# Optimization experiments

Measured on AMD Instinct MI355X. Metric: run time of the kernel, lower is better.

Reference implementation:

```python
import jax, jax.numpy as jnp
import numpy as np

ALPHA = 2.0    # ATan surrogate sharpness
V_TH = 1.0     # LIF firing threshold
TAU = 2.0      # LIF membrane time constant
BN_EPS = 1e-5
NUM_HEADS = 8

@jax.custom_vjp
def spike(u):
    return (u >= 0.0).astype(u.dtype)

def _spike_fwd(u):
    return spike(u), u

def _spike_bwd(u, g):
    s = (jnp.pi / 2.0) * ALPHA * u
    return (g * (ALPHA / 2.0) / (1.0 + s * s),)

spike.defvjp(_spike_fwd, _spike_bwd)

def lif(x):
    # x: (T, ...) -> binary spikes, multi-step LIF with hard reset
    def step(mem, xt):
        mem = mem + (xt - mem) / TAU
        s = spike(mem - V_TH)
        return mem * (1.0 - s), s
    _, out = jax.lax.scan(step, jnp.zeros_like(x[0]), x)
    return out

def bn_eval(y, bn):
    g, be, m, v = bn[0], bn[1], bn[2], bn[3]  # each (C,)
    return (y - m) * jax.lax.rsqrt(v + BN_EPS) * g + be

def linear_bn_lif(x, W, b, bn):
    # x: (T,B,N,C); W: (C_out, C_in) torch convention
    y = jnp.einsum('tbnc,dc->tbnd', x, W) + b
    return lif(bn_eval(y, bn))

def setup_inputs() -> dict:
    key = jax.random.key(0)
    ks = jax.random.split(key, 6)
    T, B, N, C = 4, 8, 1024, 512
    scale = 1.0 / np.sqrt(C)
    x = jax.random.normal(ks[0], (T, B, N, C), dtype=jnp.float32)
    Wq = jax.random.normal(ks[1], (C, C), dtype=jnp.float32) * scale
    Wk = jax.random.normal(ks[2], (C, C), dtype=jnp.float32) * scale
    Wv = jax.random.normal(ks[3], (C, C), dtype=jnp.float32) * scale
    Wp = jax.random.normal(ks[4], (C, C), dtype=jnp.float32) * scale
    zeros = jnp.zeros((C,), dtype=jnp.float32)
    ones = jnp.ones((C,), dtype=jnp.float32)
    # bn_params[l] = (gamma, beta, running_mean, running_var) for q_bn,k_bn,v_bn,proj_bn
    bn_one = jnp.stack([ones, zeros, zeros, ones])  # (4, C)
    bn_params = jnp.tile(bn_one[None], (4, 1, 1))   # (4, 4, C)
    return {"x": x, "Wq": Wq, "bq": zeros, "Wk": Wk, "bk": zeros,
            "Wv": Wv, "bv": zeros, "Wp": Wp, "bp": zeros, "bn_params": bn_params}

def reference(x, Wq, bq, Wk, bk, Wv, bv, Wp, bp, bn_params):
    T, B, N, C = x.shape
    H = NUM_HEADS
    D = C // H
    q = linear_bn_lif(x, Wq, bq, bn_params[0])
    k = linear_bn_lif(x, Wk, bk, bn_params[1])
    v = linear_bn_lif(x, Wv, bv, bn_params[2])
    # (T,B,N,C) -> (T,B,H,N,D)
    q = q.reshape(T, B, N, H, D).transpose(0, 1, 3, 2, 4)
    k = k.reshape(T, B, N, H, D).transpose(0, 1, 3, 2, 4)
    v = v.reshape(T, B, N, H, D).transpose(0, 1, 3, 2, 4)
    # attention_linear variant: kv = (k^T @ v) / n; y = q @ kv
    # SparseMatmul's tile-sparsity fallback computes the same dense matmul math.
    kv = jnp.einsum('tbhnd,tbhne->tbhde', k, v) / float(N)
    y = jnp.einsum('tbhnd,tbhde->tbhne', q, kv)
    y = y.transpose(0, 1, 3, 2, 4).reshape(T, B, N, C)
    y = lif(y)  # attn_lif
    # final projection: proj -> proj_bn -> proj_lif
    y = jnp.einsum('tbnc,dc->tbnd', y, Wp) + bp
    y = bn_eval(y, bn_params[3])
    y = lif(y)  # proj_lif
    return y
```

## Files before the change

kernel.cpp:

```cpp
#include <hip/hip_runtime.h>
#include <hip/hip_bf16.h>

constexpr int T_ = 4, B_ = 8, N_ = 1024, C_ = 512, H_ = 8, D_ = 64;
constexpr int M_ = B_ * N_;
constexpr int MT_ = T_ * M_;
constexpr int K_ = 512;

#define TAU_INV 0.5f
#define V_TH    1.0f
#define BN_EPS  1e-5f

__device__ __forceinline__ void ld4(const float* p, float* d) {
  const float4 v = *(const float4*)p;
  d[0] = v.x; d[1] = v.y; d[2] = v.z; d[3] = v.w;
}
__device__ __forceinline__ void ld4(const __hip_bfloat16* p, float* d) {
  const ushort4 u = *(const ushort4*)p;
  d[0] = __bfloat162float(*(const __hip_bfloat16*)&u.x);
  d[1] = __bfloat162float(*(const __hip_bfloat16*)&u.y);
  d[2] = __bfloat162float(*(const __hip_bfloat16*)&u.z);
  d[3] = __bfloat162float(*(const __hip_bfloat16*)&u.w);
}
__device__ __forceinline__ void st4(__hip_bfloat16* p, const float* s) {
  ushort4 u;
  *(__hip_bfloat16*)&u.x = __float2bfloat16(s[0]);
  *(__hip_bfloat16*)&u.y = __float2bfloat16(s[1]);
  *(__hip_bfloat16*)&u.z = __float2bfloat16(s[2]);
  *(__hip_bfloat16*)&u.w = __float2bfloat16(s[3]);
  *(ushort4*)p = u;
}
__device__ __forceinline__ void st4(float* p, const float* s) {
  *(float4*)p = make_float4(s[0], s[1], s[2], s[3]);
}

template <typename TIn>
__global__ __launch_bounds__(256, 2) void gemm_bn(
    const TIn* __restrict__ A, const float* __restrict__ W,
    const float* __restrict__ bias, const float* __restrict__ bnp,
    float* __restrict__ Y)
{
  constexpr int BK = 32;
  __shared__ __align__(16) float As[BK][128 + 4];
  __shared__ __align__(16) float Bs[BK][256 + 8];

  const int tid = threadIdx.x;
  const int tx = tid & 15, ty = tid >> 4;
  const int bm = blockIdx.y * 128;
  const int bn0 = blockIdx.x * 256;

  float acc[2][4][4][4];
#pragma unroll
  for (int g = 0; g < 2; ++g)
#pragma unroll
    for (int h = 0; h < 4; ++h)
#pragma unroll
      for (int i = 0; i < 4; ++i)
#pragma unroll
        for (int j = 0; j < 4; ++j) acc[g][h][i][j] = 0.0f;

  for (int k0 = 0; k0 < K_; k0 += BK) {
#pragma unroll
    for (int i = 0; i < 4; ++i) {
      const int idx = tid + 256 * i;
      const int row = idx >> 3, q = idx & 7;
      float tmp[4];
      ld4(&A[(size_t)(bm + row) * K_ + k0 + q * 4], tmp);
#pragma unroll
      for (int j = 0; j < 4; ++j) As[q * 4 + j][row] = tmp[j];
    }
#pragma unroll
    for (int i = 0; i < 8; ++i) {
      const int idx = tid + 256 * i;
      const int n = idx >> 3, q = idx & 7;
      float tmp[4];
      ld4(&W[(size_t)(bn0 + n) * K_ + k0 + q * 4], tmp);
#pragma unroll
      for (int j = 0; j < 4; ++j) Bs[q * 4 + j][n] = tmp[j];
    }
    __syncthreads();

#pragma unroll
    for (int kk = 0; kk < BK; ++kk) {
      float a[2][4], b[4][4];
#pragma unroll
      for (int g = 0; g < 2; ++g)
        ld4(&As[kk][ty * 4 + g * 64], a[g]);
#pragma unroll
      for (int h = 0; h < 4; ++h)
        ld4(&Bs[kk][tx * 4 + h * 64], b[h]);
#pragma unroll
      for (int g = 0; g < 2; ++g)
#pragma unroll
        for (int h = 0; h < 4; ++h)
#pragma unroll
          for (int i = 0; i < 4; ++i)
#pragma unroll
            for (int j = 0; j < 4; ++j)
              acc[g][h][i][j] += a[g][i] * b[h][j];
    }
    __syncthreads();
  }

#pragma unroll
  for (int h = 0; h < 4; ++h) {
    const int dl = tx * 4 + h * 64;
    const int d = bn0 + dl;
    float bi[4], gg[4], be[4], mu[4], vv[4];
    ld4(&bias[d], bi);
    ld4(&bnp[d], gg);
    ld4(&bnp[C_ + d], be);
    ld4(&bnp[2 * C_ + d], mu);
    ld4(&bnp[3 * C_ + d], vv);
    float inv[4];
#pragma unroll
    for (int j = 0; j < 4; ++j) inv[j] = 1.0f / sqrtf(vv[j] + BN_EPS);
#pragma unroll
    for (int g = 0; g < 2; ++g)
#pragma unroll
      for (int i = 0; i < 4; ++i) {
        const int row = bm + ty * 4 + g * 64 + i;
        float sv[4];
#pragma unroll
        for (int j = 0; j < 4; ++j) {
          float y = acc[g][h][i][j] + bi[j];
          y = (y - mu[j]) * inv[j] * gg[j] + be[j];
          sv[j] = y;
        }
        st4(&Y[(size_t)row * C_ + d], sv);
      }
  }
}

template <typename TOut>
__global__ __launch_bounds__(256) void lif_scan(
    const float* __restrict__ Y, TOut* __restrict__ S)
{
  const size_t npt = (size_t)M_ * C_;
  const size_t idx4 = ((size_t)blockIdx.x * 256 + threadIdx.x) * 4;
  if (idx4 >= npt) return;
  float mem[4] = {0.0f, 0.0f, 0.0f, 0.0f};
#pragma unroll
  for (int t = 0; t < T_; ++t) {
    float y[4], sv[4];
    ld4(&Y[(size_t)t * npt + idx4], y);
#pragma unroll
    for (int j = 0; j < 4; ++j) {
      float m2 = mem[j] + (y[j] - mem[j]) * TAU_INV;
      float s = (m2 - V_TH >= 0.0f) ? 1.0f : 0.0f;
      sv[j] = s;
      mem[j] = (s != 0.0f) ? 0.0f : m2;
    }
    st4(&S[(size_t)t * npt + idx4], sv);
  }
}

__global__ __launch_bounds__(256) void attn_kernel(
    const __hip_bfloat16* __restrict__ Q,
    const __hip_bfloat16* __restrict__ Kk,
    const __hip_bfloat16* __restrict__ V,
    float* __restrict__ Y)
{
  __shared__ float s1[64][65];
  __shared__ float s2[64][65];
  __shared__ float kv[64][65];
  const int tid = threadIdx.x;
  const int h = blockIdx.x, b = blockIdx.y, t = blockIdx.z;
  const size_t base = ((size_t)t * B_ + b) * (size_t)N_ * C_ + (size_t)h * D_;
  const int d0 = (tid >> 4) * 4;
  const int e0 = (tid & 15) * 4;

  float acc[4][4];
#pragma unroll
  for (int i = 0; i < 4; ++i)
#pragma unroll
    for (int j = 0; j < 4; ++j) acc[i][j] = 0.0f;

  for (int nc = 0; nc < N_; nc += 64) {
#pragma unroll
    for (int i = 0; i < 16; ++i) {
      int idx = tid + i * 256;
      int r = idx >> 6, c = idx & 63;
      s1[r][c] = __bfloat162float(Kk[base + (size_t)(nc + r) * C_ + c]);
      s2[r][c] = __bfloat162float(V[base + (size_t)(nc + r) * C_ + c]);
    }
    __syncthreads();
#pragma unroll
    for (int nn = 0; nn < 64; ++nn) {
      float a[4], bb[4];
#pragma unroll
      for (int i = 0; i < 4; ++i) a[i] = s1[nn][d0 + i];
#pragma unroll
      for (int j = 0; j < 4; ++j) bb[j] = s2[nn][e0 + j];
#pragma unroll
      for (int i = 0; i < 4; ++i)
#pragma unroll
        for (int j = 0; j < 4; ++j) acc[i][j] += a[i] * bb[j];
    }
    __syncthreads();
  }
#pragma unroll
  for (int i = 0; i < 4; ++i)
#pragma unroll
    for (int j = 0; j < 4; ++j)
      kv[d0 + i][e0 + j] = acc[i][j] * (1.0f / (float)N_);
  __syncthreads();

  for (int rc = 0; rc < N_; rc += 64) {
#pragma unroll
    for (int i = 0; i < 16; ++i) {
      int idx = tid + i * 256;
      int r = idx >> 6, c = idx & 63;
      s1[r][c] = __bfloat162float(Q[base + (size_t)(rc + r) * C_ + c]);
    }
    __syncthreads();
    float o[4][4];
#pragma unroll
    for (int i = 0; i < 4; ++i)
#pragma unroll
      for (int j = 0; j < 4; ++j) o[i][j] = 0.0f;
#pragma unroll
    for (int d = 0; d < 64; ++d) {
      float a[4], bb[4];
#pragma unroll
      for (int i = 0; i < 4; ++i) a[i] = s1[d0 + i][d];
#pragma unroll
      for (int j = 0; j < 4; ++j) bb[j] = kv[d][e0 + j];
#pragma unroll
      for (int i = 0; i < 4; ++i)
#pragma unroll
        for (int j = 0; j < 4; ++j) o[i][j] += a[i] * bb[j];
    }
#pragma unroll
    for (int i = 0; i < 4; ++i)
#pragma unroll
      for (int j = 0; j < 4; ++j)
        Y[base + (size_t)(rc + d0 + i) * C_ + e0 + j] = o[i][j];
    __syncthreads();
  }
}

extern "C" void kernel_launch(void* const* d_in, const int* in_sizes, int n_in,
                              void* d_out, int out_size, void* d_ws, size_t ws_size,
                              hipStream_t stream)
{
  const float* x   = (const float*)d_in[0];
  const float* Wq  = (const float*)d_in[1];
  const float* bq  = (const float*)d_in[2];
  const float* Wk  = (const float*)d_in[3];
  const float* bk  = (const float*)d_in[4];
  const float* Wv  = (const float*)d_in[5];
  const float* bv  = (const float*)d_in[6];
  const float* Wp  = (const float*)d_in[7];
  const float* bp  = (const float*)d_in[8];
  const float* bnp = (const float*)d_in[9];
  float* out = (float*)d_out;

  char* ws = (char*)d_ws;
  const size_t nElem = (size_t)T_ * M_ * C_;
  float*          Y   = (float*)ws;          ws += nElem * sizeof(float);
  __hip_bfloat16* q_s = (__hip_bfloat16*)ws; ws += nElem * sizeof(__hip_bfloat16);
  __hip_bfloat16* k_s = (__hip_bfloat16*)ws; ws += nElem * sizeof(__hip_bfloat16);
  __hip_bfloat16* v_s = (__hip_bfloat16*)ws; ws += nElem * sizeof(__hip_bfloat16);
  __hip_bfloat16* a_s = (__hip_bfloat16*)ws; ws += nElem * sizeof(__hip_bfloat16);

  const dim3 gg(C_ / 256, MT_ / 128);
  const unsigned lif_grid = (unsigned)(((size_t)M_ * C_ / 4 + 255) / 256);

  gemm_bn<float><<<gg, 256, 0, stream>>>(x, Wq, bq, bnp + 0 * 4 * C_, Y);
  lif_scan<__hip_bfloat16><<<lif_grid, 256, 0, stream>>>(Y, q_s);
  gemm_bn<float><<<gg, 256, 0, stream>>>(x, Wk, bk, bnp + 1 * 4 * C_, Y);
  lif_scan<__hip_bfloat16><<<lif_grid, 256, 0, stream>>>(Y, k_s);
  gemm_bn<float><<<gg, 256, 0, stream>>>(x, Wv, bv, bnp + 2 * 4 * C_, Y);
  lif_scan<__hip_bfloat16><<<lif_grid, 256, 0, stream>>>(Y, v_s);

  attn_kernel<<<dim3(H_, B_, T_), 256, 0, stream>>>(q_s, k_s, v_s, Y);
  lif_scan<__hip_bfloat16><<<lif_grid, 256, 0, stream>>>(Y, a_s);

  gemm_bn<__hip_bfloat16><<<gg, 256, 0, stream>>>(a_s, Wp, bp, bnp + 3 * 4 * C_, Y);
  lif_scan<float><<<lif_grid, 256, 0, stream>>>(Y, out);
}
```

Measured before the change: 1.178 ms.

## Batch Q/K/V GEMMs into one launch over row halves with swizzled shared tiles

The Q, K and V projections now run as one GEMM launch, with blockIdx.z picking the weight, done in two halves over the M rows so the float staging buffer stays smaller. A fused LIF kernel then scans all three outputs per half. The GEMM tile K depth drops from 32 to 16 with an XOR swizzle on the shared-memory column layout to cut bank conflicts, and launch bounds allow 3 blocks per SM. This cuts the number of launches and improves occupancy and x reuse across the three weights. The cost is a larger workspace (3x half-size Y) and more K-loop iterations with syncs.

```diff
diff --git a/kernel.cpp b/kernel.cpp
--- a/kernel.cpp
+++ b/kernel.cpp
@@ -3,8 +3,8 @@
 
 constexpr int T_ = 4, B_ = 8, N_ = 1024, C_ = 512, H_ = 8, D_ = 64;
 constexpr int M_ = B_ * N_;
-constexpr int MT_ = T_ * M_;
 constexpr int K_ = 512;
+constexpr int MH_ = 4096;
 
 #define TAU_INV 0.5f
 #define V_TH    1.0f
@@ -33,21 +33,39 @@
   *(float4*)p = make_float4(s[0], s[1], s[2], s[3]);
 }
 
-template <typename TIn>
-__global__ __launch_bounds__(256, 2) void gemm_bn(
-    const TIn* __restrict__ A, const float* __restrict__ W,
-    const float* __restrict__ bias, const float* __restrict__ bnp,
-    float* __restrict__ Y)
-{
-  constexpr int BK = 32;
-  __shared__ __align__(16) float As[BK][128 + 4];
-  __shared__ __align__(16) float Bs[BK][256 + 8];
+template <typename TIn> struct GemmArgs {
+  const TIn* A;
+  const float* W[3];
+  const float* bias[3];
+  const float* bn[3];
+  float* Y[3];
+  int half_base;
+};
+
+template <int RSHIFT, typename TIn>
+__global__ __launch_bounds__(256, 3) void gemm_bn(GemmArgs<TIn> args)
+{
+  constexpr int BK = 16;
+  constexpr int RMASK = (1 << RSHIFT) - 1;
+  __shared__ __align__(16) float AsF[BK * 132];
+  __shared__ __align__(16) float BsF[BK * 260];
+
+  const int w = blockIdx.z;
+  const TIn*   __restrict__ A    = args.A;
+  const float* __restrict__ W    = args.W[w];
+  const float* __restrict__ bias = args.bias[w];
+  const float* __restrict__ bnp  = args.bn[w];
+  float*       __restrict__ Y    = args.Y[w];
+  const int halfb = args.half_base;
 
   const int tid = threadIdx.x;
   const int tx = tid & 15, ty = tid >> 4;
   const int bm = blockIdx.y * 128;
   const int bn0 = blockIdx.x * 256;
 
+  const float* Ard[2] = { AsF + (ty ^ 0) * 4, AsF + (ty ^ 1) * 4 };
+  const float* Brd[2] = { BsF + (tx ^ 0) * 4, BsF + (tx ^ 1) * 4 };
+
   float acc[2][4][4][4];
 #pragma unroll
   for (int g = 0; g < 2; ++g)
@@ -59,35 +77,40 @@
         for (int j = 0; j < 4; ++j) acc[g][h][i][j] = 0.0f;
 
   for (int k0 = 0; k0 < K_; k0 += BK) {
+#pragma unroll
+    for (int i = 0; i < 2; ++i) {
+      const int idx = tid + 256 * i;
+      const int m = idx >> 2, q = idx & 3;
+      const int r = bm + m;
+      const size_t arow = (size_t)(r >> RSHIFT) * M_ + halfb + (r & RMASK);
+      float tmp[4];
+      ld4(&A[arow * K_ + k0 + q * 4], tmp);
+      const int colb = (((m >> 2) ^ (q >> 1)) << 2) + (m & 3);
+#pragma unroll
+      for (int j = 0; j < 4; ++j) AsF[(4 * q + j) * 132 + colb] = tmp[j];
+    }
 #pragma unroll
     for (int i = 0; i < 4; ++i) {
       const int idx = tid + 256 * i;
-      const int row = idx >> 3, q = idx & 7;
-      float tmp[4];
-      ld4(&A[(size_t)(bm + row) * K_ + k0 + q * 4], tmp);
-#pragma unroll
-      for (int j = 0; j < 4; ++j) As[q * 4 + j][row] = tmp[j];
-    }
-#pragma unroll
-    for (int i = 0; i < 8; ++i) {
-      const int idx = tid + 256 * i;
-      const int n = idx >> 3, q = idx & 7;
+      const int n = idx >> 2, q = idx & 3;
       float tmp[4];
       ld4(&W[(size_t)(bn0 + n) * K_ + k0 + q * 4], tmp);
-#pragma unroll
-      for (int j = 0; j < 4; ++j) Bs[q * 4 + j][n] = tmp[j];
+      const int colb = (((n >> 2) ^ (q >> 1)) << 2) + (n & 3);
+#pragma unroll
+      for (int j = 0; j < 4; ++j) BsF[(4 * q + j) * 260 + colb] = tmp[j];
     }
     __syncthreads();
 
 #pragma unroll
     for (int kk = 0; kk < BK; ++kk) {
+      const int s = kk >> 3;
       float a[2][4], b[4][4];
 #pragma unroll
       for (int g = 0; g < 2; ++g)
-        ld4(&As[kk][ty * 4 + g * 64], a[g]);
+        ld4(Ard[s] + kk * 132 + 64 * g, a[g]);
 #pragma unroll
       for (int h = 0; h < 4; ++h)
-        ld4(&Bs[kk][tx * 4 + h * 64], b[h]);
+        ld4(Brd[s] + kk * 260 + 64 * h, b[h]);
 #pragma unroll
       for (int g = 0; g < 2; ++g)
 #pragma unroll
@@ -103,8 +126,7 @@
 
 #pragma unroll
   for (int h = 0; h < 4; ++h) {
-    const int dl = tx * 4 + h * 64;
-    const int d = bn0 + dl;
+    const int d = bn0 + tx * 4 + h * 64;
     float bi[4], gg[4], be[4], mu[4], vv[4];
     ld4(&bias[d], bi);
     ld4(&bnp[d], gg);
@@ -118,7 +140,7 @@
     for (int g = 0; g < 2; ++g)
 #pragma unroll
       for (int i = 0; i < 4; ++i) {
-        const int row = bm + ty * 4 + g * 64 + i;
+        const int r = bm + ty * 4 + g * 64 + i;
         float sv[4];
 #pragma unroll
         for (int j = 0; j < 4; ++j) {
@@ -126,8 +148,38 @@
           y = (y - mu[j]) * inv[j] * gg[j] + be[j];
           sv[j] = y;
         }
-        st4(&Y[(size_t)row * C_ + d], sv);
+        st4(&Y[(size_t)r * C_ + d], sv);
       }
+  }
+}
+
+struct Lif3Args { __hip_bfloat16* S[3]; };
+
+__global__ __launch_bounds__(256) void lif3_scan(
+    const float* __restrict__ Yh, Lif3Args args, size_t half_elem_base)
+{
+  const size_t NH = (size_t)MH_ * C_;
+  const size_t npt = (size_t)M_ * C_;
+  const size_t e4 = ((size_t)blockIdx.x * 256 + threadIdx.x) * 4;
+  if (e4 >= NH) return;
+#pragma unroll
+  for (int w = 0; w < 3; ++w) {
+    __hip_bfloat16* __restrict__ S = args.S[w];
+    const float* __restrict__ Yw = Yh + (size_t)w * T_ * NH;
+    float mem[4] = {0.0f, 0.0f, 0.0f, 0.0f};
+#pragma unroll
+    for (int t = 0; t < T_; ++t) {
+      float y[4], sv[4];
+      ld4(&Yw[(size_t)t * NH + e4], y);
+#pragma unroll
+      for (int j = 0; j < 4; ++j) {
+        float m2 = mem[j] + (y[j] - mem[j]) * TAU_INV;
+        float s = (m2 - V_TH >= 0.0f) ? 1.0f : 0.0f;
+        sv[j] = s;
+        mem[j] = (s != 0.0f) ? 0.0f : m2;
+      }
+      st4(&S[(size_t)t * npt + half_elem_base + e4], sv);
+    }
   }
 }
 
@@ -257,25 +309,45 @@
 
   char* ws = (char*)d_ws;
   const size_t nElem = (size_t)T_ * M_ * C_;
-  float*          Y   = (float*)ws;          ws += nElem * sizeof(float);
+  const size_t NHT   = (size_t)T_ * MH_ * C_;
+  float*          Yh  = (float*)ws;          ws += 3 * NHT * sizeof(float);
   __hip_bfloat16* q_s = (__hip_bfloat16*)ws; ws += nElem * sizeof(__hip_bfloat16);
   __hip_bfloat16* k_s = (__hip_bfloat16*)ws; ws += nElem * sizeof(__hip_bfloat16);
   __hip_bfloat16* v_s = (__hip_bfloat16*)ws; ws += nElem * sizeof(__hip_bfloat16);
   __hip_bfloat16* a_s = (__hip_bfloat16*)ws; ws += nElem * sizeof(__hip_bfloat16);
-
-  const dim3 gg(C_ / 256, MT_ / 128);
-  const unsigned lif_grid = (unsigned)(((size_t)M_ * C_ / 4 + 255) / 256);
-
-  gemm_bn<float><<<gg, 256, 0, stream>>>(x, Wq, bq, bnp + 0 * 4 * C_, Y);
-  lif_scan<__hip_bfloat16><<<lif_grid, 256, 0, stream>>>(Y, q_s);
-  gemm_bn<float><<<gg, 256, 0, stream>>>(x, Wk, bk, bnp + 1 * 4 * C_, Y);
-  lif_scan<__hip_bfloat16><<<lif_grid, 256, 0, stream>>>(Y, k_s);
-  gemm_bn<float><<<gg, 256, 0, stream>>>(x, Wv, bv, bnp + 2 * 4 * C_, Y);
-  lif_scan<__hip_bfloat16><<<lif_grid, 256, 0, stream>>>(Y, v_s);
-
-  attn_kernel<<<dim3(H_, B_, T_), 256, 0, stream>>>(q_s, k_s, v_s, Y);
-  lif_scan<__hip_bfloat16><<<lif_grid, 256, 0, stream>>>(Y, a_s);
-
-  gemm_bn<__hip_bfloat16><<<gg, 256, 0, stream>>>(a_s, Wp, bp, bnp + 3 * 4 * C_, Y);
-  lif_scan<float><<<lif_grid, 256, 0, stream>>>(Y, out);
-}
+  float* Yfull = (float*)Yh;
+
+  GemmArgs<float> qa;
+  qa.A = x;
+  qa.W[0] = Wq; qa.W[1] = Wk; qa.W[2] = Wv;
+  qa.bias[0] = bq; qa.bias[1] = bk; qa.bias[2] = bv;
+  qa.bn[0] = bnp + 0 * 4 * C_;
+  qa.bn[1] = bnp + 1 * 4 * C_;
+  qa.bn[2] = bnp + 2 * 4 * C_;
+  qa.Y[0] = Yh; qa.Y[1] = Yh + NHT; qa.Y[2] = Yh + 2 * NHT;
+
+  Lif3Args la; la.S[0] = q_s; la.S[1] = k_s; la.S[2] = v_s;
+
+  const dim3 ggq(C_ / 256, (T_ * MH_) / 128, 3);
+  const unsigned lif3_grid = (unsigned)(((size_t)MH_ * C_ / 4 + 255) / 256);
+  const unsigned lif_grid  = (unsigned)(((size_t)M_ * C_ / 4 + 255) / 256);
+
+  qa.half_base = 0;
+  gemm_bn<12, float><<<ggq, 256, 0, stream>>>(qa);
+  lif3_scan<<<lif3_grid, 256, 0, stream>>>(Yh, la, 0);
+
+  qa.half_base = MH_;
+  gemm_bn<12, float><<<ggq, 256, 0, stream>>>(qa);
+  lif3_scan<<<lif3_grid, 256, 0, stream>>>(Yh, la, (size_t)MH_ * C_);
+
+  attn_kernel<<<dim3(H_, B_, T_), 256, 0, stream>>>(q_s, k_s, v_s, Yfull);
+  lif_scan<__hip_bfloat16><<<lif_grid, 256, 0, stream>>>(Yfull, a_s);
+
+  GemmArgs<__hip_bfloat16> pa;
+  pa.A = a_s;
+  pa.W[0] = Wp;  pa.bias[0] = bp;  pa.bn[0] = bnp + 3 * 4 * C_;
+  pa.Y[0] = Yfull;
+  pa.half_base = 0;
+  gemm_bn<13, __hip_bfloat16><<<dim3(C_ / 256, (T_ * M_) / 128, 1), 256, 0, stream>>>(pa);
+  lif_scan<float><<<lif_grid, 256, 0, stream>>>(Yfull, out);
+}
```

After: 3.840 ms. 226% more time.

## Fuse LIF scan into GEMM epilogue with time-interleaved transposed layout and LDS DMA

Applied to the files above, without the earlier changes.

The input and weights are pre-transposed so that each GEMM tile holds all four timesteps of a row group. The LIF recurrence can then run inside the GEMM epilogue, which removes the fp32 intermediate Y round-trips and the separate lif_scan launches. The q/k/v GEMMs are merged into one launch along the z dimension. Tiles are loaded with global_load_lds DMA instead of register-staged transposed stores. Two transpose kernels are added, and the attention output LIF now writes a transposed bf16 layout for the projection GEMM.

```diff
diff --git a/kernel.cpp b/kernel.cpp
--- a/kernel.cpp
+++ b/kernel.cpp
@@ -2,8 +2,8 @@
 #include <hip/hip_bf16.h>
 
 constexpr int T_ = 4, B_ = 8, N_ = 1024, C_ = 512, H_ = 8, D_ = 64;
-constexpr int M_ = B_ * N_;
-constexpr int MT_ = T_ * M_;
+constexpr int M_ = 8192;
+constexpr int MT_ = 32768;
 constexpr int K_ = 512;
 
 #define TAU_INV 0.5f
@@ -33,20 +33,83 @@
   *(float4*)p = make_float4(s[0], s[1], s[2], s[3]);
 }
 
-template <typename TIn>
-__global__ __launch_bounds__(256, 2) void gemm_bn(
-    const TIn* __restrict__ A, const float* __restrict__ W,
-    const float* __restrict__ bias, const float* __restrict__ bnp,
-    float* __restrict__ Y)
+__device__ __forceinline__ void dma16(const void* g, void* l) {
+  __builtin_amdgcn_global_load_lds(
+      (const __attribute__((address_space(1))) unsigned int*)g,
+      (__attribute__((address_space(3))) unsigned int*)l, 16, 0, 0);
+}
+
+struct WPtrs { const float* W[4]; };
+
+__global__ __launch_bounds__(256) void transpose_w(WPtrs wp, float* __restrict__ Wt)
+{
+  __shared__ float tile[32][33];
+  const int w = blockIdx.z;
+  const float* __restrict__ W = wp.W[w];
+  float* __restrict__ dst = Wt + (size_t)w * K_ * C_;
+  const int k0 = blockIdx.x * 32, d0 = blockIdx.y * 32;
+  const int tx = threadIdx.x, ty = threadIdx.y;
+#pragma unroll
+  for (int i = 0; i < 32; i += 8)
+    tile[ty + i][tx] = W[(size_t)(d0 + ty + i) * K_ + k0 + tx];
+  __syncthreads();
+#pragma unroll
+  for (int i = 0; i < 32; i += 8)
+    dst[(size_t)(k0 + ty + i) * C_ + d0 + tx] = tile[tx][ty + i];
+}
+
+__global__ __launch_bounds__(256) void transpose_x(
+    const float* __restrict__ x, float* __restrict__ XT)
+{
+  __shared__ float tile[32][132];
+  const int bk = blockIdx.x * 32, bm = blockIdx.y * 32;
+  const int tx = threadIdx.x & 31, ty = threadIdx.x >> 5;
+#pragma unroll
+  for (int t = 0; t < T_; ++t)
+#pragma unroll
+    for (int i = 0; i < 4; ++i) {
+      const int m = ty + 8 * i;
+      tile[tx][m * 4 + t] = x[((size_t)t * M_ + bm + m) * K_ + bk + tx];
+    }
+  __syncthreads();
+  const int k = threadIdx.x >> 3, q = threadIdx.x & 7;
+#pragma unroll
+  for (int u = 0; u < 4; ++u)
+    st4(&XT[(size_t)(bk + k) * MT_ + bm * 4 + q * 16 + u * 4],
+        &tile[k][q * 16 + u * 4]);
+}
+
+template <typename TIn, typename TOut>
+struct GArgs {
+  const TIn* AT;
+  const float* Wt[3];
+  const float* bias[3];
+  const float* bn[3];
+  TOut* S[3];
+};
+
+template <typename TIn, typename TOut>
+__global__ __launch_bounds__(256, 2) void gemm_lif(GArgs<TIn, TOut> args)
 {
   constexpr int BK = 32;
-  __shared__ __align__(16) float As[BK][128 + 4];
-  __shared__ __align__(16) float Bs[BK][256 + 8];
-
-  const int tid = threadIdx.x;
+  constexpr bool BF = (sizeof(TIn) == 2);
+  __shared__ __align__(16) TIn  As[BK * 128];
+  __shared__ __align__(16) float Bs[BK * 256];
+
+  const int z = blockIdx.z;
+  const TIn*   __restrict__ AT   = args.AT;
+  const float* __restrict__ Wt   = args.Wt[z];
+  const float* __restrict__ bias = args.bias[z];
+  const float* __restrict__ bnp  = args.bn[z];
+  TOut*        __restrict__ S    = args.S[z];
+
+  const int tid  = threadIdx.x;
+  const int lane = tid & 63;
+  const int wave = __builtin_amdgcn_readfirstlane(tid >> 6);
   const int tx = tid & 15, ty = tid >> 4;
-  const int bm = blockIdx.y * 128;
-  const int bn0 = blockIdx.x * 256;
+  const int bm_m = blockIdx.y * 32;
+  const int bm4  = bm_m * 4;
+  const int bn0  = blockIdx.x * 256;
 
   float acc[2][4][4][4];
 #pragma unroll
@@ -59,23 +122,28 @@
         for (int j = 0; j < 4; ++j) acc[g][h][i][j] = 0.0f;
 
   for (int k0 = 0; k0 < K_; k0 += BK) {
-#pragma unroll
-    for (int i = 0; i < 4; ++i) {
-      const int idx = tid + 256 * i;
-      const int row = idx >> 3, q = idx & 7;
-      float tmp[4];
-      ld4(&A[(size_t)(bm + row) * K_ + k0 + q * 4], tmp);
-#pragma unroll
-      for (int j = 0; j < 4; ++j) As[q * 4 + j][row] = tmp[j];
-    }
-#pragma unroll
-    for (int i = 0; i < 8; ++i) {
-      const int idx = tid + 256 * i;
-      const int n = idx >> 3, q = idx & 7;
-      float tmp[4];
-      ld4(&W[(size_t)(bn0 + n) * K_ + k0 + q * 4], tmp);
-#pragma unroll
-      for (int j = 0; j < 4; ++j) Bs[q * 4 + j][n] = tmp[j];
+    if constexpr (!BF) {
+#pragma unroll
+      for (int c = 0; c < 4; ++c) {
+        const int ins = wave * 4 + c;
+        const int kk = ins * 2 + (lane >> 5);
+        dma16(AT + (size_t)(k0 + kk) * MT_ + bm4 + (lane & 31) * 4,
+              (void*)((float*)As + ins * 256));
+      }
+    } else {
+#pragma unroll
+      for (int c = 0; c < 2; ++c) {
+        const int ins = wave * 2 + c;
+        const int kk = ins * 4 + (lane >> 4);
+        dma16(AT + (size_t)(k0 + kk) * MT_ + bm4 + (lane & 15) * 8,
+              (void*)((TIn*)As + ins * 512));
+      }
+    }
+#pragma unroll
+    for (int c = 0; c < 8; ++c) {
+      const int ins = wave * 8 + c;
+      dma16(Wt + (size_t)(k0 + ins) * C_ + bn0 + lane * 4,
+            (void*)(Bs + ins * 256));
     }
     __syncthreads();
 
@@ -84,10 +152,10 @@
       float a[2][4], b[4][4];
 #pragma unroll
       for (int g = 0; g < 2; ++g)
-        ld4(&As[kk][ty * 4 + g * 64], a[g]);
+        ld4((const TIn*)As + kk * 128 + ty * 4 + 64 * g, a[g]);
 #pragma unroll
       for (int h = 0; h < 4; ++h)
-        ld4(&Bs[kk][tx * 4 + h * 64], b[h]);
+        ld4(Bs + kk * 256 + tx * 4 + 64 * h, b[h]);
 #pragma unroll
       for (int g = 0; g < 2; ++g)
 #pragma unroll
@@ -103,8 +171,7 @@
 
 #pragma unroll
   for (int h = 0; h < 4; ++h) {
-    const int dl = tx * 4 + h * 64;
-    const int d = bn0 + dl;
+    const int d = bn0 + tx * 4 + 64 * h;
     float bi[4], gg[4], be[4], mu[4], vv[4];
     ld4(&bias[d], bi);
     ld4(&bnp[d], gg);
@@ -115,43 +182,53 @@
 #pragma unroll
     for (int j = 0; j < 4; ++j) inv[j] = 1.0f / sqrtf(vv[j] + BN_EPS);
 #pragma unroll
-    for (int g = 0; g < 2; ++g)
-#pragma unroll
-      for (int i = 0; i < 4; ++i) {
-        const int row = bm + ty * 4 + g * 64 + i;
-        float sv[4];
-#pragma unroll
-        for (int j = 0; j < 4; ++j) {
-          float y = acc[g][h][i][j] + bi[j];
+    for (int g = 0; g < 2; ++g) {
+      const int m = bm_m + ty + 16 * g;
+      float sv[4][4];
+#pragma unroll
+      for (int j = 0; j < 4; ++j) {
+        float mm = 0.0f;
+#pragma unroll
+        for (int t = 0; t < 4; ++t) {
+          float y = acc[g][h][t][j] + bi[j];
           y = (y - mu[j]) * inv[j] * gg[j] + be[j];
-          sv[j] = y;
+          float m2 = mm + (y - mm) * TAU_INV;
+          float s = (m2 - V_TH >= 0.0f) ? 1.0f : 0.0f;
+          sv[t][j] = s;
+          mm = (s != 0.0f) ? 0.0f : m2;
         }
-        st4(&Y[(size_t)row * C_ + d], sv);
       }
-  }
-}
-
-template <typename TOut>
-__global__ __launch_bounds__(256) void lif_scan(
-    const float* __restrict__ Y, TOut* __restrict__ S)
-{
-  const size_t npt = (size_t)M_ * C_;
-  const size_t idx4 = ((size_t)blockIdx.x * 256 + threadIdx.x) * 4;
-  if (idx4 >= npt) return;
+#pragma unroll
+      for (int t = 0; t < 4; ++t)
+        st4(&S[((size_t)t * M_ + m) * C_ + d], sv[t]);
+    }
+  }
+}
+
+__global__ __launch_bounds__(256) void lif_T(
+    const float* __restrict__ Y, __hip_bfloat16* __restrict__ AT)
+{
+  __shared__ __hip_bfloat16 lds[64][72];
+  const int bm = blockIdx.x * 16, bc = blockIdx.y * 64;
+  const int tid = threadIdx.x;
+  const int mm = tid >> 4, c4 = (tid & 15) * 4;
   float mem[4] = {0.0f, 0.0f, 0.0f, 0.0f};
 #pragma unroll
   for (int t = 0; t < T_; ++t) {
-    float y[4], sv[4];
-    ld4(&Y[(size_t)t * npt + idx4], y);
+    float y[4];
+    ld4(&Y[((size_t)t * M_ + bm + mm) * C_ + bc + c4], y);
 #pragma unroll
     for (int j = 0; j < 4; ++j) {
       float m2 = mem[j] + (y[j] - mem[j]) * TAU_INV;
       float s = (m2 - V_TH >= 0.0f) ? 1.0f : 0.0f;
-      sv[j] = s;
+      lds[c4 + j][mm * 4 + t] = __float2bfloat16(s);
       mem[j] = (s != 0.0f) ? 0.0f : m2;
     }
-    st4(&S[(size_t)t * npt + idx4], sv);
-  }
+  }
+  __syncthreads();
+  const int c = tid >> 2, q = tid & 3;
+  *(uint4*)(AT + (size_t)(bc + c) * MT_ + bm * 4 + q * 16) =
+      *(const uint4*)&lds[c][q * 16];
 }
 
 __global__ __launch_bounds__(256) void attn_kernel(
@@ -256,26 +333,38 @@
   float* out = (float*)d_out;
 
   char* ws = (char*)d_ws;
-  const size_t nElem = (size_t)T_ * M_ * C_;
-  float*          Y   = (float*)ws;          ws += nElem * sizeof(float);
-  __hip_bfloat16* q_s = (__hip_bfloat16*)ws; ws += nElem * sizeof(__hip_bfloat16);
-  __hip_bfloat16* k_s = (__hip_bfloat16*)ws; ws += nElem * sizeof(__hip_bfloat16);
-  __hip_bfloat16* v_s = (__hip_bfloat16*)ws; ws += nElem * sizeof(__hip_bfloat16);
-  __hip_bfloat16* a_s = (__hip_bfloat16*)ws; ws += nElem * sizeof(__hip_bfloat16);
-
-  const dim3 gg(C_ / 256, MT_ / 128);
-  const unsigned lif_grid = (unsigned)(((size_t)M_ * C_ / 4 + 255) / 256);
-
-  gemm_bn<float><<<gg, 256, 0, stream>>>(x, Wq, bq, bnp + 0 * 4 * C_, Y);
-  lif_scan<__hip_bfloat16><<<lif_grid, 256, 0, stream>>>(Y, q_s);
-  gemm_bn<float><<<gg, 256, 0, stream>>>(x, Wk, bk, bnp + 1 * 4 * C_, Y);
-  lif_scan<__hip_bfloat16><<<lif_grid, 256, 0, stream>>>(Y, k_s);
-  gemm_bn<float><<<gg, 256, 0, stream>>>(x, Wv, bv, bnp + 2 * 4 * C_, Y);
-  lif_scan<__hip_bfloat16><<<lif_grid, 256, 0, stream>>>(Y, v_s);
+  float* XT = (float*)ws;  ws += (size_t)K_ * MT_ * sizeof(float);
+  float* Wt = (float*)ws;  ws += (size_t)4 * K_ * C_ * sizeof(float);
+  __hip_bfloat16* q_s = (__hip_bfloat16*)ws; ws += (size_t)MT_ * C_ * 2;
+  __hip_bfloat16* k_s = (__hip_bfloat16*)ws; ws += (size_t)MT_ * C_ * 2;
+  __hip_bfloat16* v_s = (__hip_bfloat16*)ws; ws += (size_t)MT_ * C_ * 2;
+  float* Y = XT;
+  __hip_bfloat16* aT = q_s;
+
+  WPtrs wp; wp.W[0] = Wq; wp.W[1] = Wk; wp.W[2] = Wv; wp.W[3] = Wp;
+  transpose_w<<<dim3(K_ / 32, C_ / 32, 4), dim3(32, 8), 0, stream>>>(wp, Wt);
+  transpose_x<<<dim3(K_ / 32, M_ / 32), 256, 0, stream>>>(x, XT);
+
+  GArgs<float, __hip_bfloat16> qa;
+  qa.AT = XT;
+  qa.Wt[0] = Wt; qa.Wt[1] = Wt + (size_t)K_ * C_; qa.Wt[2] = Wt + (size_t)2 * K_ * C_;
+  qa.bias[0] = bq; qa.bias[1] = bk; qa.bias[2] = bv;
+  qa.bn[0] = bnp + 0 * 4 * C_;
+  qa.bn[1] = bnp + 1 * 4 * C_;
+  qa.bn[2] = bnp + 2 * 4 * C_;
+  qa.S[0] = q_s; qa.S[1] = k_s; qa.S[2] = v_s;
+  gemm_lif<float, __hip_bfloat16>
+      <<<dim3(C_ / 256, M_ / 32, 3), 256, 0, stream>>>(qa);
 
   attn_kernel<<<dim3(H_, B_, T_), 256, 0, stream>>>(q_s, k_s, v_s, Y);
-  lif_scan<__hip_bfloat16><<<lif_grid, 256, 0, stream>>>(Y, a_s);
-
-  gemm_bn<__hip_bfloat16><<<gg, 256, 0, stream>>>(a_s, Wp, bp, bnp + 3 * 4 * C_, Y);
-  lif_scan<float><<<lif_grid, 256, 0, stream>>>(Y, out);
-}
+  lif_T<<<dim3(M_ / 16, C_ / 64), 256, 0, stream>>>(Y, aT);
+
+  GArgs<__hip_bfloat16, float> pa;
+  pa.AT = aT;
+  pa.Wt[0] = Wt + (size_t)3 * K_ * C_;
+  pa.bias[0] = bp;
+  pa.bn[0] = bnp + 3 * 4 * C_;
+  pa.S[0] = out;
+  gemm_lif<__hip_bfloat16, float>
+      <<<dim3(C_ / 256, M_ / 32, 1), 256, 0, stream>>>(pa);
+}
```

New measurement: 984.4 us. -16.4%, faster.
